# Optimization experiments

Measured on AMD Instinct MI355X. Metric: run time of the kernel, lower is better.

Reference implementation:

```python
import jax, jax.numpy as jnp
from jax import lax
import numpy as np

DIM = 384
HEADS = 8
MLP_HIDDEN = int(DIM * 4.0)
EPS = 1e-5


def layer_norm(x, g, b):
    m = jnp.mean(x, axis=-1, keepdims=True)
    v = jnp.mean((x - m) ** 2, axis=-1, keepdims=True)
    return (x - m) * lax.rsqrt(v + EPS) * g + b


def conv_pos_enc(x, H, W, w, b):
    # x: (B, N, C) -> depthwise 3x3 conv residual, act=Identity (cpe_act=False)
    B, N, C = x.shape
    feat = jnp.transpose(x, (0, 2, 1)).reshape(B, C, H, W)
    feat = lax.conv_general_dilated(
        feat, w, window_strides=(1, 1), padding='SAME',
        feature_group_count=C, dimension_numbers=('NCHW', 'OIHW', 'NCHW'))
    feat = feat + b[None, :, None, None]
    feat = jnp.transpose(feat.reshape(B, C, N), (0, 2, 1))
    return x + feat


def channel_attn(x, qkv_w, proj_w, proj_b):
    B, N, C = x.shape
    h = HEADS
    hd = C // h
    scale = hd ** (-0.5)
    qkv = x @ qkv_w.T                                # (B, N, 3C)
    qkv = qkv.reshape(B, N, 3, h, hd)
    qkv = jnp.transpose(qkv, (2, 0, 3, 1, 4))        # (3, B, h, N, hd)
    q, k, v = qkv[0], qkv[1], qkv[2]
    k = k * scale
    attn = jnp.einsum('bhnd,bhne->bhde', k, v)       # (B, h, hd, hd)
    attn = jax.nn.softmax(attn, axis=-1)
    out = jnp.einsum('bhde,bhne->bhnd', attn, q)     # (B, h, N, hd)
    out = jnp.transpose(out, (0, 2, 1, 3)).reshape(B, N, C)
    return out @ proj_w.T + proj_b


def mlp(x, fc1_w, fc1_b, fc2_w, fc2_b):
    h = jax.nn.gelu(x @ fc1_w.T + fc1_b, approximate=False)
    return h @ fc2_w.T + fc2_b


def setup_inputs() -> dict:
    key = jax.random.key(0)
    ks = jax.random.split(key, 12)
    C, Hd = DIM, MLP_HIDDEN
    s = 0.02
    return {
        'x': jax.random.normal(ks[0], (32, 784, C), dtype=jnp.float32),
        'H': 28,
        'W': 28,
        'cpe0_w': jax.random.normal(ks[1], (C, 1, 3, 3), dtype=jnp.float32) * s,
        'cpe0_b': jnp.zeros((C,), dtype=jnp.float32),
        'cpe1_w': jax.random.normal(ks[2], (C, 1, 3, 3), dtype=jnp.float32) * s,
        'cpe1_b': jnp.zeros((C,), dtype=jnp.float32),
        'norm1_g': jnp.ones((C,), dtype=jnp.float32),
        'norm1_b': jnp.zeros((C,), dtype=jnp.float32),
        'qkv_w': jax.random.normal(ks[3], (3 * C, C), dtype=jnp.float32) * s,
        'proj_w': jax.random.normal(ks[4], (C, C), dtype=jnp.float32) * s,
        'proj_b': jnp.zeros((C,), dtype=jnp.float32),
        'norm2_g': jnp.ones((C,), dtype=jnp.float32),
        'norm2_b': jnp.zeros((C,), dtype=jnp.float32),
        'fc1_w': jax.random.normal(ks[5], (Hd, C), dtype=jnp.float32) * s,
        'fc1_b': jnp.zeros((Hd,), dtype=jnp.float32),
        'fc2_w': jax.random.normal(ks[6], (C, Hd), dtype=jnp.float32) * s,
        'fc2_b': jnp.zeros((C,), dtype=jnp.float32),
    }


def reference(x, H, W, cpe0_w, cpe0_b, cpe1_w, cpe1_b, norm1_g, norm1_b,
              qkv_w, proj_w, proj_b, norm2_g, norm2_b,
              fc1_w, fc1_b, fc2_w, fc2_b):
    x = conv_pos_enc(x, H, W, cpe0_w, cpe0_b)
    cur = layer_norm(x, norm1_g, norm1_b)
    x = x + channel_attn(cur, qkv_w, proj_w, proj_b)
    x = conv_pos_enc(x, H, W, cpe1_w, cpe1_b)
    x = x + mlp(layer_norm(x, norm2_g, norm2_b), fc1_w, fc1_b, fc2_w, fc2_b)
    return x
```

## Files before the change

### kernel.cpp

```cpp
#include <hip/hip_runtime.h>
#include <hip/hip_bf16.h>
#include <math.h>
#include <stdint.h>

#define B_     32
#define HH_    28
#define WW_    28
#define N_     784
#define C_     384
#define M_     25088
#define HEADS_ 8
#define HD_    48
#define HID_   1536

typedef __bf16 bf16;
typedef __attribute__((ext_vector_type(8))) __bf16 bf16x8;
typedef __attribute__((ext_vector_type(4))) __bf16 bf16x4;
typedef __attribute__((ext_vector_type(4))) float f32x4;

__device__ __forceinline__ void gload_lds16(const void* g, void* l) {
    __builtin_amdgcn_global_load_lds(
        (const __attribute__((address_space(1))) unsigned int*)g,
        (__attribute__((address_space(3))) unsigned int*)(uintptr_t)l,
        16, 0, 0);
}

__global__ void convert4_kernel(const float* __restrict__ a, int na,
                                const float* __restrict__ b, int nb,
                                const float* __restrict__ c, int nc,
                                const float* __restrict__ d, int nd,
                                bf16* __restrict__ out) {
    int i = blockIdx.x * 256 + threadIdx.x;
    int j = i;
    const float* src;
    if (j < na) src = a + j;
    else { j -= na;
        if (j < nb) src = b + j;
        else { j -= nb;
            if (j < nc) src = c + j;
            else { j -= nc;
                if (j >= nd) return;
                src = d + j; } } }
    out[i] = (bf16)(*src);
}

__global__ void wtrans_kernel(const float* __restrict__ w0, const float* __restrict__ w1,
                              float* __restrict__ wt0, float* __restrict__ wt1) {
    int i = blockIdx.x * 256 + threadIdx.x;
    if (i >= C_ * 9) return;
    int c = i / 9, t = i - c * 9;
    wt0[t * C_ + c] = w0[i];
    wt1[t * C_ + c] = w1[i];
}

__global__ __launch_bounds__(256)
void cpe_ln_kernel(const float* __restrict__ x, const float* __restrict__ wt,
                   const float* __restrict__ bias, float* __restrict__ y,
                   const float* __restrict__ g, const float* __restrict__ beta,
                   bf16* __restrict__ lnout) {
    const int wave = threadIdx.x >> 6, lane = threadIdx.x & 63;
    const int f = blockIdx.x;
    const int row = (f & 7) * 3136 + (f >> 3) * 4 + wave;
    const int b = row / N_;
    const int n = row - b * N_;
    const int py = n / WW_, px = n - py * WW_;

    float acc[6], ctr[6];
    const float* xrow = x + (size_t)row * C_ + lane;
    #pragma unroll
    for (int j = 0; j < 6; j++) {
        acc[j] = bias[lane + j * 64];
        ctr[j] = xrow[j * 64];
    }

    if (py >= 1 && py <= 26 && px >= 1 && px <= 26) {
        const float* p = x + (size_t)(row - WW_ - 1) * C_ + lane;
        float v[9][6];
        #pragma unroll
        for (int t = 0; t < 9; t++) {
            if (t == 4) continue;
            const float* pt = p + ((t / 3) * WW_ + (t % 3)) * C_;
            #pragma unroll
            for (int j = 0; j < 6; j++) v[t][j] = pt[j * 64];
        }
        #pragma unroll
        for (int t = 0; t < 9; t++) {
            #pragma unroll
            for (int j = 0; j < 6; j++) {
                float xv = (t == 4) ? ctr[j] : v[t][j];
                acc[j] += wt[t * C_ + lane + j * 64] * xv;
            }
        }
    } else {
        #pragma unroll
        for (int t = 0; t < 9; t++) {
            int yy = py + t / 3 - 1, xx = px + t % 3 - 1;
            if (yy < 0 || yy >= HH_ || xx < 0 || xx >= WW_) continue;
            const float* pt = x + (size_t)(b * N_ + yy * WW_ + xx) * C_ + lane;
            #pragma unroll
            for (int j = 0; j < 6; j++)
                acc[j] += wt[t * C_ + lane + j * 64] * pt[j * 64];
        }
    }
    #pragma unroll
    for (int j = 0; j < 6; j++) acc[j] += ctr[j];

    float* yrow = y + (size_t)row * C_ + lane;
    #pragma unroll
    for (int j = 0; j < 6; j++) yrow[j * 64] = acc[j];

    float s = 0.f;
    #pragma unroll
    for (int j = 0; j < 6; j++) s += acc[j];
    #pragma unroll
    for (int off = 1; off < 64; off <<= 1) s += __shfl_xor(s, off, 64);
    float mean = s * (1.f / C_);
    float d[6], vs = 0.f;
    #pragma unroll
    for (int j = 0; j < 6; j++) { d[j] = acc[j] - mean; vs += d[j] * d[j]; }
    #pragma unroll
    for (int off = 1; off < 64; off <<= 1) vs += __shfl_xor(vs, off, 64);
    float rstd = rsqrtf(vs * (1.f / C_) + 1e-5f);
    bf16* lrow = lnout + (size_t)row * C_ + lane;
    #pragma unroll
    for (int j = 0; j < 6; j++) {
        int c = lane + j * 64;
        lrow[j * 64] = (bf16)(d[j] * rstd * g[c] + beta[c]);
    }
}

template<bool BIAS, bool GELU, bool RESID, bool OUTBF>
__global__ __launch_bounds__(256)
void gemm_kernel(const bf16* __restrict__ A, const bf16* __restrict__ Wt,
                 const float* __restrict__ bias, const float* __restrict__ resid,
                 void* __restrict__ outp, int M, int N, int K) {
    __shared__ __align__(16) bf16 As[3 * 4096];
    __shared__ __align__(16) bf16 Bs[3 * 4096];

    const int nbn = gridDim.x, nbm = gridDim.y;
    const int f = blockIdx.y * nbn + blockIdx.x;
    const int grp = f / (8 * nbn);
    const int rem = f - grp * 8 * nbn;
    const int rows = min(8, nbm - grp * 8);
    const int bm = (grp * 8 + rem % rows) * 128;
    const int bn = (rem / rows) * 128;

    const int t = threadIdx.x;
    const int wave = t >> 6, lane = t & 63;
    const int wm = (wave & 1) * 64, wn = (wave >> 1) * 64;
    const int quad = lane >> 4, r = lane & 15;

    const int ldrow = lane >> 2;
    const int ldcol = (lane & 3) * 8;
    const bf16* ga0 = A  + (size_t)(bm + wave * 32 + ldrow) * K + ldcol;
    const bf16* ga1 = ga0 + (size_t)16 * K;
    const bf16* gb0 = Wt + (size_t)(bn + wave * 32 + ldrow) * K + ldcol;
    const bf16* gb1 = gb0 + (size_t)16 * K;
    const int lbase = wave * 32 * 32;

    f32x4 acc[4][4] = {};

    gload_lds16(ga0, &As[lbase]);
    gload_lds16(ga1, &As[lbase + 512]);
    gload_lds16(gb0, &Bs[lbase]);
    gload_lds16(gb1, &Bs[lbase + 512]);
    gload_lds16(ga0 + 32, &As[4096 + lbase]);
    gload_lds16(ga1 + 32, &As[4096 + lbase + 512]);
    gload_lds16(gb0 + 32, &Bs[4096 + lbase]);
    gload_lds16(gb1 + 32, &Bs[4096 + lbase + 512]);

    int buf = 0;
    int k0 = 0;
    for (; k0 < K - 32; k0 += 32) {
        asm volatile("s_waitcnt vmcnt(4)" ::: "memory");
        asm volatile("s_barrier" ::: "memory");
        if (k0 + 64 < K) {
            const int nb3 = (buf == 0 ? 2 : buf - 1) * 4096;
            gload_lds16(ga0 + k0 + 64, &As[nb3 + lbase]);
            gload_lds16(ga1 + k0 + 64, &As[nb3 + lbase + 512]);
            gload_lds16(gb0 + k0 + 64, &Bs[nb3 + lbase]);
            gload_lds16(gb1 + k0 + 64, &Bs[nb3 + lbase + 512]);
        }
        const bf16* as = &As[buf * 4096];
        const bf16* bs = &Bs[buf * 4096];
        bf16x8 af[4], bfr[4];
        #pragma unroll
        for (int i = 0; i < 4; i++)
            af[i] = *(const bf16x8*)(&as[(wm + i * 16 + r) * 32 + quad * 8]);
        #pragma unroll
        for (int j = 0; j < 4; j++)
            bfr[j] = *(const bf16x8*)(&bs[(wn + j * 16 + r) * 32 + quad * 8]);
        #pragma unroll
        for (int i = 0; i < 4; i++)
            #pragma unroll
            for (int j = 0; j < 4; j++)
                acc[i][j] = __builtin_amdgcn_mfma_f32_16x16x32_bf16(af[i], bfr[j], acc[i][j], 0, 0, 0);
        buf = (buf == 2) ? 0 : buf + 1;
    }
    {
        asm volatile("s_waitcnt vmcnt(0)" ::: "memory");
        asm volatile("s_barrier" ::: "memory");
        const bf16* as = &As[buf * 4096];
        const bf16* bs = &Bs[buf * 4096];
        bf16x8 af[4], bfr[4];
        #pragma unroll
        for (int i = 0; i < 4; i++)
            af[i] = *(const bf16x8*)(&as[(wm + i * 16 + r) * 32 + quad * 8]);
        #pragma unroll
        for (int j = 0; j < 4; j++)
            bfr[j] = *(const bf16x8*)(&bs[(wn + j * 16 + r) * 32 + quad * 8]);
        #pragma unroll
        for (int i = 0; i < 4; i++)
            #pragma unroll
            for (int j = 0; j < 4; j++)
                acc[i][j] = __builtin_amdgcn_mfma_f32_16x16x32_bf16(af[i], bfr[j], acc[i][j], 0, 0, 0);
    }

    #pragma unroll
    for (int i = 0; i < 4; i++) {
        #pragma unroll
        for (int j = 0; j < 4; j++) {
            int n = bn + wn + j * 16 + r;
            float bv = BIAS ? bias[n] : 0.f;
            #pragma unroll
            for (int e = 0; e < 4; e++) {
                int m = bm + wm + i * 16 + quad * 4 + e;
                float val = acc[i][j][e] + bv;
                if (GELU) val = 0.5f * val * (1.f + erff(val * 0.70710678118654752f));
                if (RESID) val += resid[(size_t)m * N + n];
                if (OUTBF) ((bf16*)outp)[(size_t)m * N + n] = (bf16)val;
                else       ((float*)outp)[(size_t)m * N + n] = val;
            }
        }
    }
}

__global__ __launch_bounds__(256)
void attn_fused_kernel(const bf16* __restrict__ qkvb, bf16* __restrict__ outp) {
    __shared__ __align__(16) bf16 stage[4][3872];
    __shared__ float Sred[4][48][49];
    __shared__ __align__(16) bf16 attn_s[48 * 72];

    const int bh = blockIdx.x;
    const int b = bh >> 3, h = bh & 7;
    const int t = threadIdx.x;
    const int wave = t >> 6, lane = t & 63;
    const int quad = lane >> 4, r = lane & 15;
    const int tensor = lane >> 5;
    const int n_local = lane & 31;

    const size_t qkv_base = (size_t)b * N_ * 1152;
    const int toff = 384 + tensor * 384 + h * 48;

    f32x4 acc[3][3] = {};
    bf16* kT = &stage[wave][0];
    bf16* vT = &stage[wave][1936];
    bf16* myT = &stage[wave][tensor * 1936];

    for (int c = wave; c < 25; c += 4) {
        int n0 = c * 32;
        bf16 rowbuf[48];
        if (n0 + n_local < N_) {
            const uint4* src = (const uint4*)(qkvb + qkv_base + (size_t)(n0 + n_local) * 1152 + toff);
            #pragma unroll
            for (int i = 0; i < 6; i++) *(uint4*)(&rowbuf[i * 8]) = src[i];
        } else {
            #pragma unroll
            for (int i = 0; i < 48; i++) rowbuf[i] = (bf16)0.f;
        }
        #pragma unroll
        for (int d = 0; d < 48; d++) myT[d * 40 + n_local] = rowbuf[d];
        bf16x8 af[3], bfv[3];
        #pragma unroll
        for (int i = 0; i < 3; i++) af[i]  = *(const bf16x8*)(&kT[(i * 16 + r) * 40 + quad * 8]);
        #pragma unroll
        for (int j = 0; j < 3; j++) bfv[j] = *(const bf16x8*)(&vT[(j * 16 + r) * 40 + quad * 8]);
        #pragma unroll
        for (int i = 0; i < 3; i++)
            #pragma unroll
            for (int j = 0; j < 3; j++)
                acc[i][j] = __builtin_amdgcn_mfma_f32_16x16x32_bf16(af[i], bfv[j], acc[i][j], 0, 0, 0);
    }

    #pragma unroll
    for (int i = 0; i < 3; i++)
        #pragma unroll
        for (int j = 0; j < 3; j++)
            #pragma unroll
            for (int e = 0; e < 4; e++)
                Sred[wave][i * 16 + quad * 4 + e][j * 16 + r] = acc[i][j][e];
    __syncthreads();

    if (t < 48) {
        float row[48];
        float mx = -1e30f;
        #pragma unroll
        for (int e = 0; e < 48; e++) {
            float s = Sred[0][t][e] + Sred[1][t][e] + Sred[2][t][e] + Sred[3][t][e];
            s *= 0.14433756729740644f;
            row[e] = s;
            mx = fmaxf(mx, s);
        }
        float sum = 0.f;
        #pragma unroll
        for (int e = 0; e < 48; e++) { float ex = __expf(row[e] - mx); row[e] = ex; sum += ex; }
        float inv = 1.f / sum;
        #pragma unroll
        for (int e = 0; e < 48; e++) attn_s[t * 72 + e] = (bf16)(row[e] * inv);
        #pragma unroll
        for (int e = 48; e < 64; e++) attn_s[t * 72 + e] = (bf16)0.f;
    }
    __syncthreads();

    const bf16* qbase = qkvb + qkv_base + h * 48;
    for (int nt = wave; nt < 49; nt += 4) {
        int n0 = nt * 16;
        f32x4 oacc[3] = {};
        #pragma unroll
        for (int kc = 0; kc < 2; kc++) {
            bf16x8 bq = *(const bf16x8*)(qbase + (size_t)(n0 + r) * 1152 + kc * 32 + quad * 8);
            #pragma unroll
            for (int i = 0; i < 3; i++) {
                bf16x8 aa = *(const bf16x8*)(&attn_s[(i * 16 + r) * 72 + kc * 32 + quad * 8]);
                oacc[i] = __builtin_amdgcn_mfma_f32_16x16x32_bf16(aa, bq, oacc[i], 0, 0, 0);
            }
        }
        #pragma unroll
        for (int i = 0; i < 3; i++) {
            bf16x4 ov;
            #pragma unroll
            for (int e = 0; e < 4; e++) ov[e] = (bf16)oacc[i][e];
            *(bf16x4*)(outp + (size_t)(b * N_ + n0 + r) * 384 + h * 48 + i * 16 + quad * 4) = ov;
        }
    }
}

extern "C" void kernel_launch(void* const* d_in, const int* in_sizes, int n_in,
                              void* d_out, int out_size, void* d_ws, size_t ws_size,
                              hipStream_t stream) {
    const float* x      = (const float*)d_in[0];
    const float* cpe0_w = (const float*)d_in[3];
    const float* cpe0_b = (const float*)d_in[4];
    const float* cpe1_w = (const float*)d_in[5];
    const float* cpe1_b = (const float*)d_in[6];
    const float* n1g    = (const float*)d_in[7];
    const float* n1b    = (const float*)d_in[8];
    const float* qkv_w  = (const float*)d_in[9];
    const float* proj_w = (const float*)d_in[10];
    const float* proj_b = (const float*)d_in[11];
    const float* n2g    = (const float*)d_in[12];
    const float* n2b    = (const float*)d_in[13];
    const float* fc1_w  = (const float*)d_in[14];
    const float* fc1_b  = (const float*)d_in[15];
    const float* fc2_w  = (const float*)d_in[16];
    const float* fc2_b  = (const float*)d_in[17];

    char* ws = (char*)d_ws;
    size_t off = 0;
    bf16* cur    = (bf16*)(ws + off); off += (size_t)M_ * C_ * 2;
    bf16* qkvb   = (bf16*)(ws + off);
    float* x3    = (float*)qkvb;
    off += (size_t)M_ * 1152 * 2;
    bf16* hbuf   = (bf16*)(ws + off); off += (size_t)M_ * HID_ * 2;
    bf16* qkv_wb  = (bf16*)(ws + off); off += (size_t)1152 * 384 * 2;
    bf16* proj_wb = (bf16*)(ws + off); off += (size_t)384 * 384 * 2;
    bf16* fc1_wb  = (bf16*)(ws + off); off += (size_t)HID_ * 384 * 2;
    bf16* fc2_wb  = (bf16*)(ws + off); off += (size_t)384 * HID_ * 2;
    float* wt0    = (float*)(ws + off); off += (size_t)C_ * 9 * 4;
    float* wt1    = (float*)(ws + off); off += (size_t)C_ * 9 * 4;
    float* out = (float*)d_out;

    const int na = 442368, nb = 147456, nc = 589824, nd = 589824;
    convert4_kernel<<<(na + nb + nc + nd + 255) / 256, 256, 0, stream>>>(
        qkv_w, na, proj_w, nb, fc1_w, nc, fc2_w, nd, qkv_wb);
    wtrans_kernel<<<(C_ * 9 + 255) / 256, 256, 0, stream>>>(cpe0_w, cpe1_w, wt0, wt1);

    cpe_ln_kernel<<<M_ / 4, 256, 0, stream>>>(x, wt0, cpe0_b, out, n1g, n1b, cur);
    gemm_kernel<false, false, false, true><<<dim3(1152 / 128, M_ / 128), 256, 0, stream>>>(
        cur, qkv_wb, nullptr, nullptr, qkvb, M_, 1152, 384);
    attn_fused_kernel<<<256, 256, 0, stream>>>(qkvb, cur);
    gemm_kernel<true, false, true, false><<<dim3(384 / 128, M_ / 128), 256, 0, stream>>>(
        cur, proj_wb, proj_b, out, out, M_, 384, 384);
    cpe_ln_kernel<<<M_ / 4, 256, 0, stream>>>(out, wt1, cpe1_b, x3, n2g, n2b, cur);
    gemm_kernel<true, true, false, true><<<dim3(HID_ / 128, M_ / 128), 256, 0, stream>>>(
        cur, fc1_wb, fc1_b, nullptr, hbuf, M_, HID_, 384);
    gemm_kernel<true, false, true, false><<<dim3(384 / 128, M_ / 128), 256, 0, stream>>>(
        hbuf, fc2_wb, fc2_b, x3, out, M_, 384, HID_);
}
```

Before: 375.6 us.

## Deepen GEMM pipeline, swizzle LDS, vectorize epilogue, use tanh GELU

Result: slower. 402.8 us (+7.3%).

```diff
diff --git a/kernel.cpp b/kernel.cpp
--- a/kernel.cpp
+++ b/kernel.cpp
@@ -23,6 +23,11 @@
         (const __attribute__((address_space(1))) unsigned int*)g,
         (__attribute__((address_space(3))) unsigned int*)(uintptr_t)l,
         16, 0, 0);
+}
+
+__device__ __forceinline__ float gelu_f(float v) {
+    float u = 0.7978845608028654f * v * (1.f + 0.044715f * v * v);
+    return __fdividef(v, 1.f + __expf(-2.f * u));
 }
 
 __global__ void convert4_kernel(const float* __restrict__ a, int na,
@@ -134,8 +139,8 @@
 void gemm_kernel(const bf16* __restrict__ A, const bf16* __restrict__ Wt,
                  const float* __restrict__ bias, const float* __restrict__ resid,
                  void* __restrict__ outp, int M, int N, int K) {
-    __shared__ __align__(16) bf16 As[3 * 4096];
-    __shared__ __align__(16) bf16 Bs[3 * 4096];
+    __shared__ __align__(16) bf16 As[4 * 4096];
+    __shared__ __align__(16) bf16 Bs[4 * 4096];
 
     const int nbn = gridDim.x, nbm = gridDim.y;
     const int f = blockIdx.y * nbn + blockIdx.x;
@@ -151,85 +156,75 @@
     const int quad = lane >> 4, r = lane & 15;
 
     const int ldrow = lane >> 2;
-    const int ldcol = (lane & 3) * 8;
+    const int ldcol = ((lane & 3) ^ ((lane >> 3) & 3)) * 8;
     const bf16* ga0 = A  + (size_t)(bm + wave * 32 + ldrow) * K + ldcol;
     const bf16* ga1 = ga0 + (size_t)16 * K;
     const bf16* gb0 = Wt + (size_t)(bn + wave * 32 + ldrow) * K + ldcol;
     const bf16* gb1 = gb0 + (size_t)16 * K;
-    const int lbase = wave * 32 * 32;
+    const int lbase = wave * 1024;
+
+    const int nk = K >> 5;
+
+    auto issue = [&](int st) {
+        const int kk = st * 32;
+        const int bb = (st & 3) * 4096;
+        gload_lds16(ga0 + kk, &As[bb + lbase]);
+        gload_lds16(ga1 + kk, &As[bb + lbase + 512]);
+        gload_lds16(gb0 + kk, &Bs[bb + lbase]);
+        gload_lds16(gb1 + kk, &Bs[bb + lbase + 512]);
+    };
 
     f32x4 acc[4][4] = {};
-
-    gload_lds16(ga0, &As[lbase]);
-    gload_lds16(ga1, &As[lbase + 512]);
-    gload_lds16(gb0, &Bs[lbase]);
-    gload_lds16(gb1, &Bs[lbase + 512]);
-    gload_lds16(ga0 + 32, &As[4096 + lbase]);
-    gload_lds16(ga1 + 32, &As[4096 + lbase + 512]);
-    gload_lds16(gb0 + 32, &Bs[4096 + lbase]);
-    gload_lds16(gb1 + 32, &Bs[4096 + lbase + 512]);
-
-    int buf = 0;
-    int k0 = 0;
-    for (; k0 < K - 32; k0 += 32) {
-        asm volatile("s_waitcnt vmcnt(4)" ::: "memory");
+    issue(0); issue(1); issue(2);
+
+    const int sq = (quad ^ ((r >> 1) & 3)) * 8;
+
+    for (int s = 0; s < nk; ++s) {
+        const int left = nk - s;
+        if (left >= 3)      asm volatile("s_waitcnt vmcnt(8)" ::: "memory");
+        else if (left == 2) asm volatile("s_waitcnt vmcnt(4)" ::: "memory");
+        else                asm volatile("s_waitcnt vmcnt(0)" ::: "memory");
         asm volatile("s_barrier" ::: "memory");
-        if (k0 + 64 < K) {
-            const int nb3 = (buf == 0 ? 2 : buf - 1) * 4096;
-            gload_lds16(ga0 + k0 + 64, &As[nb3 + lbase]);
-            gload_lds16(ga1 + k0 + 64, &As[nb3 + lbase + 512]);
-            gload_lds16(gb0 + k0 + 64, &Bs[nb3 + lbase]);
-            gload_lds16(gb1 + k0 + 64, &Bs[nb3 + lbase + 512]);
-        }
-        const bf16* as = &As[buf * 4096];
-        const bf16* bs = &Bs[buf * 4096];
+        if (s + 3 < nk) issue(s + 3);
+
+        const bf16* as = &As[(s & 3) * 4096];
+        const bf16* bs = &Bs[(s & 3) * 4096];
         bf16x8 af[4], bfr[4];
         #pragma unroll
         for (int i = 0; i < 4; i++)
-            af[i] = *(const bf16x8*)(&as[(wm + i * 16 + r) * 32 + quad * 8]);
+            af[i] = *(const bf16x8*)(&as[(wm + i * 16 + r) * 32 + sq]);
         #pragma unroll
         for (int j = 0; j < 4; j++)
-            bfr[j] = *(const bf16x8*)(&bs[(wn + j * 16 + r) * 32 + quad * 8]);
+            bfr[j] = *(const bf16x8*)(&bs[(wn + j * 16 + r) * 32 + sq]);
         #pragma unroll
         for (int i = 0; i < 4; i++)
             #pragma unroll
             for (int j = 0; j < 4; j++)
-                acc[i][j] = __builtin_amdgcn_mfma_f32_16x16x32_bf16(af[i], bfr[j], acc[i][j], 0, 0, 0);
-        buf = (buf == 2) ? 0 : buf + 1;
-    }
-    {
-        asm volatile("s_waitcnt vmcnt(0)" ::: "memory");
-        asm volatile("s_barrier" ::: "memory");
-        const bf16* as = &As[buf * 4096];
-        const bf16* bs = &Bs[buf * 4096];
-        bf16x8 af[4], bfr[4];
-        #pragma unroll
-        for (int i = 0; i < 4; i++)
-            af[i] = *(const bf16x8*)(&as[(wm + i * 16 + r) * 32 + quad * 8]);
-        #pragma unroll
-        for (int j = 0; j < 4; j++)
-            bfr[j] = *(const bf16x8*)(&bs[(wn + j * 16 + r) * 32 + quad * 8]);
-        #pragma unroll
-        for (int i = 0; i < 4; i++)
-            #pragma unroll
-            for (int j = 0; j < 4; j++)
-                acc[i][j] = __builtin_amdgcn_mfma_f32_16x16x32_bf16(af[i], bfr[j], acc[i][j], 0, 0, 0);
-    }
-
-    #pragma unroll
-    for (int i = 0; i < 4; i++) {
-        #pragma unroll
-        for (int j = 0; j < 4; j++) {
-            int n = bn + wn + j * 16 + r;
-            float bv = BIAS ? bias[n] : 0.f;
-            #pragma unroll
-            for (int e = 0; e < 4; e++) {
-                int m = bm + wm + i * 16 + quad * 4 + e;
-                float val = acc[i][j][e] + bv;
-                if (GELU) val = 0.5f * val * (1.f + erff(val * 0.70710678118654752f));
-                if (RESID) val += resid[(size_t)m * N + n];
-                if (OUTBF) ((bf16*)outp)[(size_t)m * N + n] = (bf16)val;
-                else       ((float*)outp)[(size_t)m * N + n] = val;
+                acc[i][j] = __builtin_amdgcn_mfma_f32_16x16x32_bf16(bfr[j], af[i], acc[i][j], 0, 0, 0);
+    }
+
+    #pragma unroll
+    for (int j = 0; j < 4; j++) {
+        const int n = bn + wn + j * 16 + quad * 4;
+        f32x4 bv = {};
+        if (BIAS) bv = *(const f32x4*)(&bias[n]);
+        #pragma unroll
+        for (int i = 0; i < 4; i++) {
+            const size_t m = (size_t)(bm + wm + i * 16 + r);
+            f32x4 v = acc[i][j];
+            if (BIAS) v += bv;
+            if (GELU) {
+                #pragma unroll
+                for (int e = 0; e < 4; e++) v[e] = gelu_f(v[e]);
+            }
+            if (RESID) v += *(const f32x4*)(&resid[m * N + n]);
+            if (OUTBF) {
+                bf16x4 ov;
+                #pragma unroll
+                for (int e = 0; e < 4; e++) ov[e] = (bf16)v[e];
+                *(bf16x4*)((bf16*)outp + m * N + n) = ov;
+            } else {
+                *(f32x4*)((float*)outp + m * N + n) = v;
             }
         }
     }
```
